# Performance work log

Measured on AMD Instinct MI355X. Metric: run time of the kernel, lower is better.

Reference implementation:

```python
import jax, jax.numpy as jnp
import numpy as np

NUM_EDGE_CLASS = 4
NODE_DIM = 64
BATCH = 8
NUM_NODES = 512


def setup_inputs() -> dict:
    key = jax.random.key(0)
    k1, k2, k3, k4, k5 = jax.random.split(key, 5)
    node_state = jax.random.normal(k1, (BATCH, NUM_NODES, NODE_DIM), dtype=jnp.float32)
    adj_mat = jax.random.randint(k2, (BATCH, NUM_NODES, NUM_NODES), 0, NUM_EDGE_CLASS, dtype=jnp.int32)
    matrix_in = jax.random.normal(k3, (NUM_EDGE_CLASS, NODE_DIM, NODE_DIM), dtype=jnp.float32) * 0.1
    matrix_out = jax.random.normal(k4, (NUM_EDGE_CLASS, NODE_DIM, NODE_DIM), dtype=jnp.float32) * 0.1
    bias = jax.random.normal(k5, (2 * NODE_DIM,), dtype=jnp.float32) * 0.1
    return {"node_state": node_state, "adj_mat": adj_mat,
            "matrix_in": matrix_in, "matrix_out": matrix_out, "bias": bias}


def reference(node_state, adj_mat, matrix_in, matrix_out, bias):
    # Original builds a_in[b,v,w] = matrix_in[adj[b,v,w]] ([B,N,N,D,D]) and a giant
    # [B, N*D, N*D] block matrix; equivalently, with one-hot over edge classes:
    #   msg_in[b,v,d]  = sum_w matrix_in[adj[b,v,w]][d,e]  * h[b,w,e]
    #   msg_out[b,v,d] = sum_w matrix_out[adj[b,w,v]][d,e] * h[b,w,e]  (transposed adj)
    oh = jax.nn.one_hot(adj_mat, matrix_in.shape[0], dtype=node_state.dtype)  # [B,V,W,C]
    msg_in = jnp.einsum('bvwc,cde,bwe->bvd', oh, matrix_in, node_state)
    msg_out = jnp.einsum('bwvc,cde,bwe->bvd', oh, matrix_out, node_state)
    return jnp.concatenate([msg_in, msg_out], axis=-1) + bias  # [B,N,2D]
```

## Files before the change

### kernel.cpp

```cpp
#include <hip/hip_runtime.h>

#define NB 8
#define NN 512
#define DD 64

typedef short bf16x8 __attribute__((ext_vector_type(8)));
typedef float f32x4 __attribute__((ext_vector_type(4)));

__device__ __forceinline__ unsigned short f2bf(float f) {
    unsigned int x = __builtin_bit_cast(unsigned int, f);
    x += 0x7FFFu + ((x >> 16) & 1u);
    return (unsigned short)(x >> 16);
}

__device__ __forceinline__ void gload_lds16(const void* g, void* lds) {
    __builtin_amdgcn_global_load_lds(
        (const __attribute__((address_space(1))) unsigned int*)g,
        (__attribute__((address_space(3))) unsigned int*)lds, 16, 0, 0);
}

__device__ __forceinline__ bf16x8 onehot_packed(unsigned int bits, unsigned int rep) {
    unsigned int x = bits ^ rep;
    unsigned int y = x | (x >> 1);
    unsigned int m = ~y & 0x55555555u;
    union { unsigned int u[4]; bf16x8 v; } r;
    #pragma unroll
    for (int j = 0; j < 4; ++j) {
        unsigned int f = m >> (4 * j);
        r.u[j] = ((f & 1u) ? 0x3F80u : 0u) | ((f & 4u) ? 0x3F800000u : 0u);
    }
    return r.v;
}

__global__ __launch_bounds__(256) void prep_kernel(
    const float* __restrict__ h, const int* __restrict__ adj,
    const float* __restrict__ Min, const float* __restrict__ Mout,
    unsigned int* __restrict__ packR, unsigned int* __restrict__ packC,
    unsigned short* __restrict__ HTbf2, unsigned short* __restrict__ Wbf)
{
    const int blk = blockIdx.x, t = threadIdx.x;
    if (blk < 512) {
        __shared__ int tile[64][65];
        const int b = blk >> 6, ti = blk & 63;
        const int tr = (ti >> 3) * 64, tc = (ti & 7) * 64;
        const int* src = adj + (size_t)b * NN * NN;
        #pragma unroll
        for (int i = 0; i < 16; ++i) {
            int idx = i * 256 + t, rr = idx >> 6, cc = idx & 63;
            tile[rr][cc] = src[(size_t)(tr + rr) * NN + tc + cc];
        }
        __syncthreads();
        {
            int r = t >> 2, g = t & 3;
            unsigned int ur = 0, uc = 0;
            #pragma unroll
            for (int j = 0; j < 16; ++j) {
                ur |= ((unsigned int)tile[r][16 * g + j] & 3u) << (2 * j);
                uc |= ((unsigned int)tile[16 * g + j][r] & 3u) << (2 * j);
            }
            packR[((size_t)b * NN + tr + r) * 32 + (tc >> 4) + g] = ur;
            packC[((size_t)b * NN + tc + r) * 32 + (tr >> 4) + g] = uc;
        }
    } else if (blk < 576) {
        __shared__ float tf[64][65];
        const int bb = blk - 512, b = bb >> 3, w0 = (bb & 7) * 64;
        #pragma unroll
        for (int i = 0; i < 16; ++i) {
            int idx = i * 256 + t, w = idx >> 6, e = idx & 63;
            tf[w][e] = h[((size_t)b * NN + w0 + w) * DD + e];
        }
        __syncthreads();
        unsigned int* HT32 = (unsigned int*)HTbf2;
        const int n = t >> 6, r = (t >> 2) & 15, p = t & 3;
        #pragma unroll
        for (int i = 0; i < 8; ++i) {
            int woct = (w0 >> 3) + i;
            int kb = woct & 3, kc = (woct >> 2) & 3, cch = woct >> 4;
            int slab = (cch * 4 + kc) * 4 + n;
            unsigned int lo = f2bf(tf[8 * i + 2 * p][n * 16 + r]);
            unsigned int hi = f2bf(tf[8 * i + 2 * p + 1][n * 16 + r]);
            HT32[(size_t)b * 16384 + slab * 256 + kb * 64 + r * 4 + p] =
                lo | (hi << 16);
        }
    } else {
        int idx = (blk - 576) * 256 + t;
        int dir = idx >> 14, d = (idx >> 8) & 63, k = idx & 255;
        int c = k >> 6, e = k & 63;
        const float* M = dir ? Mout : Min;
        Wbf[idx] = f2bf(M[(c * DD + d) * DD + e]);
    }
}

__global__ __launch_bounds__(256) void msg_mfma_kernel(
    const unsigned int* __restrict__ packR, const unsigned int* __restrict__ packC,
    const unsigned short* __restrict__ HTbf2, const unsigned short* __restrict__ Wbf,
    const float* __restrict__ bias, float* __restrict__ out)
{
    __shared__ unsigned short HTX[64][512];
    __shared__ unsigned short S2[2][8][256];

    const int t = threadIdx.x;
    const int lane = t & 63, wv = t >> 6;
    const int dir = wv >> 1, rt = wv & 1;
    const int b = blockIdx.x >> 6;
    const int v0 = (blockIdx.x & 63) * 8;
    const int r = lane & 15, kb = lane >> 4;

    const unsigned short* HTg = HTbf2 + (size_t)b * 32768;

    #pragma unroll
    for (int q = 0; q < 16; ++q) {
        int s = wv * 16 + q;
        gload_lds16(HTg + (size_t)s * 512 + lane * 8, &HTX[s][0]);
    }

    const int vloc = rt * 4 + (r >> 2);
    const unsigned int rep = (unsigned int)(r & 3) * 0x55555555u;
    const unsigned short* prow = (const unsigned short*)(
        (dir ? packC : packR) + ((size_t)b * NN + v0 + vloc) * 32);
    unsigned int bits0  = prow[kb];        unsigned int bits1  = prow[4 + kb];
    unsigned int bits2  = prow[8 + kb];    unsigned int bits3  = prow[12 + kb];
    unsigned int bits4  = prow[16 + kb];   unsigned int bits5  = prow[20 + kb];
    unsigned int bits6  = prow[24 + kb];   unsigned int bits7  = prow[28 + kb];
    unsigned int bits8  = prow[32 + kb];   unsigned int bits9  = prow[36 + kb];
    unsigned int bits10 = prow[40 + kb];   unsigned int bits11 = prow[44 + kb];
    unsigned int bits12 = prow[48 + kb];   unsigned int bits13 = prow[52 + kb];
    unsigned int bits14 = prow[56 + kb];   unsigned int bits15 = prow[60 + kb];

    __syncthreads();

    f32x4 acc[4] = {f32x4{0,0,0,0}, f32x4{0,0,0,0}, f32x4{0,0,0,0}, f32x4{0,0,0,0}};
    #pragma unroll
    for (int c = 0; c < 4; ++c) {
        #pragma unroll
        for (int kc = 0; kc < 4; ++kc) {
            unsigned int bits;
            switch (c * 4 + kc) {
                case 0:  bits = bits0;  break;  case 1:  bits = bits1;  break;
                case 2:  bits = bits2;  break;  case 3:  bits = bits3;  break;
                case 4:  bits = bits4;  break;  case 5:  bits = bits5;  break;
                case 6:  bits = bits6;  break;  case 7:  bits = bits7;  break;
                case 8:  bits = bits8;  break;  case 9:  bits = bits9;  break;
                case 10: bits = bits10; break;  case 11: bits = bits11; break;
                case 12: bits = bits12; break;  case 13: bits = bits13; break;
                case 14: bits = bits14; break;  default: bits = bits15; break;
            }
            bf16x8 afrag = onehot_packed(bits, rep);
            #pragma unroll
            for (int n = 0; n < 4; ++n) {
                bf16x8 bfrag = *(const bf16x8*)&HTX[(c * 4 + kc) * 4 + n][lane * 8];
                acc[n] = __builtin_amdgcn_mfma_f32_16x16x32_bf16(afrag, bfrag, acc[n], 0, 0, 0);
            }
        }
    }

    #pragma unroll
    for (int ct = 0; ct < 4; ++ct) {
        #pragma unroll
        for (int rg = 0; rg < 4; ++rg) {
            int row_g = rt * 16 + kb * 4 + rg;
            int vv = row_g >> 2, cc2 = row_g & 3;
            int e = ct * 16 + r;
            int rb = (cc2 * 128 + e * 2) ^ ((vv & 7) << 4);
            *(unsigned short*)((char*)&S2[dir][vv][0] + rb) = f2bf(acc[ct][rg]);
        }
    }
    __syncthreads();

    f32x4 acc2[2] = {f32x4{0,0,0,0}, f32x4{0,0,0,0}};
    #pragma unroll
    for (int kc = 0; kc < 8; ++kc) {
        int vv = r & 7;
        int kbase = kc * 32 + kb * 8;
        int rb = (kbase * 2) ^ (vv << 4);
        bf16x8 a2 = *(const bf16x8*)((const char*)&S2[dir][vv][0] + rb);
        #pragma unroll
        for (int j = 0; j < 2; ++j) {
            int d = (rt * 2 + j) * 16 + r;
            bf16x8 b2 = *(const bf16x8*)&Wbf[(dir * DD + d) * 256 + kbase];
            acc2[j] = __builtin_amdgcn_mfma_f32_16x16x32_bf16(a2, b2, acc2[j], 0, 0, 0);
        }
    }
    #pragma unroll
    for (int j = 0; j < 2; ++j) {
        int d = (rt * 2 + j) * 16 + r;
        float bs = bias[dir * DD + d];
        #pragma unroll
        for (int rg = 0; rg < 4; ++rg) {
            int row = kb * 4 + rg;
            if (row < 8)
                out[((size_t)(b * NN + v0 + row)) * (2 * DD) + dir * DD + d] = acc2[j][rg] + bs;
        }
    }
}

__global__ __launch_bounds__(256) void msg_kernel(
    const float* __restrict__ h, const int* __restrict__ adj,
    const float* __restrict__ Min, const float* __restrict__ Mout,
    const float* __restrict__ bias, float* __restrict__ out)
{
    __shared__ __align__(16) float S[4][2][4][DD];
    const int lane = threadIdx.x & 63, wslot = threadIdx.x >> 6;
    const int wid = blockIdx.x * 4 + wslot;
    const int b = wid >> 9, v = wid & (NN - 1);
    const float* hb = h + (size_t)b * NN * DD;
    const int* adjb = adj + (size_t)b * NN * NN;
    float tot = 0.f, ain1 = 0.f, ain2 = 0.f, ain3 = 0.f, aout1 = 0.f, aout2 = 0.f, aout3 = 0.f;
    for (int w0 = 0; w0 < NN; w0 += 64) {
        int cin_chunk = adjb[v * NN + (w0 + lane)];
        int cout_chunk = adjb[(w0 + lane) * NN + v];
        #pragma unroll
        for (int k = 0; k < 64; ++k) {
            float hw = hb[(w0 + k) * DD + lane];
            int cin = __builtin_amdgcn_readlane(cin_chunk, k);
            int cout = __builtin_amdgcn_readlane(cout_chunk, k);
            tot += hw;
            ain1 = fmaf((cin == 1) ? 1.f : 0.f, hw, ain1);
            ain2 = fmaf((cin == 2) ? 1.f : 0.f, hw, ain2);
            ain3 = fmaf((cin == 3) ? 1.f : 0.f, hw, ain3);
            aout1 = fmaf((cout == 1) ? 1.f : 0.f, hw, aout1);
            aout2 = fmaf((cout == 2) ? 1.f : 0.f, hw, aout2);
            aout3 = fmaf((cout == 3) ? 1.f : 0.f, hw, aout3);
        }
    }
    S[wslot][0][0][lane] = tot - ain1 - ain2 - ain3;
    S[wslot][0][1][lane] = ain1; S[wslot][0][2][lane] = ain2; S[wslot][0][3][lane] = ain3;
    S[wslot][1][0][lane] = tot - aout1 - aout2 - aout3;
    S[wslot][1][1][lane] = aout1; S[wslot][1][2][lane] = aout2; S[wslot][1][3][lane] = aout3;
    __syncthreads();
    float o_in = 0.f, o_out = 0.f;
    #pragma unroll
    for (int c = 0; c < 4; ++c)
        for (int e0 = 0; e0 < DD; e0 += 4) {
            float4 mi = *reinterpret_cast<const float4*>(&Min[(c * DD + lane) * DD + e0]);
            float4 mo = *reinterpret_cast<const float4*>(&Mout[(c * DD + lane) * DD + e0]);
            float4 si = *reinterpret_cast<const float4*>(&S[wslot][0][c][e0]);
            float4 so = *reinterpret_cast<const float4*>(&S[wslot][1][c][e0]);
            o_in = fmaf(mi.x, si.x, fmaf(mi.y, si.y, fmaf(mi.z, si.z, fmaf(mi.w, si.w, o_in))));
            o_out = fmaf(mo.x, so.x, fmaf(mo.y, so.y, fmaf(mo.z, so.z, fmaf(mo.w, so.w, o_out))));
        }
    float* ov = out + (size_t)(b * NN + v) * (2 * DD);
    ov[lane] = o_in + bias[lane];
    ov[DD + lane] = o_out + bias[DD + lane];
}

extern "C" void kernel_launch(void* const* d_in, const int* in_sizes, int n_in,
                              void* d_out, int out_size, void* d_ws, size_t ws_size,
                              hipStream_t stream) {
    const float* node_state = (const float*)d_in[0];
    const int*   adj_mat    = (const int*)  d_in[1];
    const float* matrix_in  = (const float*)d_in[2];
    const float* matrix_out = (const float*)d_in[3];
    const float* bias       = (const float*)d_in[4];
    float* out = (float*)d_out;

    const size_t PACKR_OFF = 0;
    const size_t PACKC_OFF = (size_t)NB * NN * 32 * 4;
    const size_t HT_OFF    = PACKC_OFF + (size_t)NB * NN * 32 * 4;
    const size_t W_OFF     = HT_OFF + (size_t)NB * DD * NN * 2;
    const size_t NEED      = W_OFF + (size_t)2 * DD * 256 * 2;

    if (ws_size < NEED) {
        msg_kernel<<<NB * NN / 4, 256, 0, stream>>>(node_state, adj_mat, matrix_in,
                                                    matrix_out, bias, out);
        return;
    }
    unsigned int*   packR = (unsigned int*)((char*)d_ws + PACKR_OFF);
    unsigned int*   packC = (unsigned int*)((char*)d_ws + PACKC_OFF);
    unsigned short* HTbf2 = (unsigned short*)((char*)d_ws + HT_OFF);
    unsigned short* Wbf   = (unsigned short*)((char*)d_ws + W_OFF);

    prep_kernel<<<704, 256, 0, stream>>>(node_state, adj_mat, matrix_in, matrix_out,
                                         packR, packC, HTbf2, Wbf);
    msg_mfma_kernel<<<NB * NN / 8, 256, 0, stream>>>(packR, packC, HTbf2, Wbf, bias, out);
}
```

Before: 20.16 us.

## Fuse adjacency bit-packing into the MFMA message kernel

```diff
diff --git a/kernel.cpp b/kernel.cpp
--- a/kernel.cpp
+++ b/kernel.cpp
@@ -33,37 +33,14 @@
 }
 
 __global__ __launch_bounds__(256) void prep_kernel(
-    const float* __restrict__ h, const int* __restrict__ adj,
+    const float* __restrict__ h,
     const float* __restrict__ Min, const float* __restrict__ Mout,
-    unsigned int* __restrict__ packR, unsigned int* __restrict__ packC,
     unsigned short* __restrict__ HTbf2, unsigned short* __restrict__ Wbf)
 {
     const int blk = blockIdx.x, t = threadIdx.x;
-    if (blk < 512) {
-        __shared__ int tile[64][65];
-        const int b = blk >> 6, ti = blk & 63;
-        const int tr = (ti >> 3) * 64, tc = (ti & 7) * 64;
-        const int* src = adj + (size_t)b * NN * NN;
-        #pragma unroll
-        for (int i = 0; i < 16; ++i) {
-            int idx = i * 256 + t, rr = idx >> 6, cc = idx & 63;
-            tile[rr][cc] = src[(size_t)(tr + rr) * NN + tc + cc];
-        }
-        __syncthreads();
-        {
-            int r = t >> 2, g = t & 3;
-            unsigned int ur = 0, uc = 0;
-            #pragma unroll
-            for (int j = 0; j < 16; ++j) {
-                ur |= ((unsigned int)tile[r][16 * g + j] & 3u) << (2 * j);
-                uc |= ((unsigned int)tile[16 * g + j][r] & 3u) << (2 * j);
-            }
-            packR[((size_t)b * NN + tr + r) * 32 + (tc >> 4) + g] = ur;
-            packC[((size_t)b * NN + tc + r) * 32 + (tr >> 4) + g] = uc;
-        }
-    } else if (blk < 576) {
+    if (blk < 64) {
         __shared__ float tf[64][65];
-        const int bb = blk - 512, b = bb >> 3, w0 = (bb & 7) * 64;
+        const int b = blk >> 3, w0 = (blk & 7) * 64;
         #pragma unroll
         for (int i = 0; i < 16; ++i) {
             int idx = i * 256 + t, w = idx >> 6, e = idx & 63;
@@ -83,7 +60,7 @@
                 lo | (hi << 16);
         }
     } else {
-        int idx = (blk - 576) * 256 + t;
+        int idx = (blk - 64) * 256 + t;
         int dir = idx >> 14, d = (idx >> 8) & 63, k = idx & 255;
         int c = k >> 6, e = k & 63;
         const float* M = dir ? Mout : Min;
@@ -92,20 +69,23 @@
 }
 
 __global__ __launch_bounds__(256) void msg_mfma_kernel(
-    const unsigned int* __restrict__ packR, const unsigned int* __restrict__ packC,
+    const int* __restrict__ adj,
     const unsigned short* __restrict__ HTbf2, const unsigned short* __restrict__ Wbf,
     const float* __restrict__ bias, float* __restrict__ out)
 {
-    __shared__ unsigned short HTX[64][512];
+    __shared__ __align__(16) unsigned short HTX[64][512];
     __shared__ unsigned short S2[2][8][256];
+    __shared__ __align__(16) unsigned int pR[8][32];
+    __shared__ __align__(16) unsigned int pC[8][32];
 
     const int t = threadIdx.x;
     const int lane = t & 63, wv = t >> 6;
     const int dir = wv >> 1, rt = wv & 1;
-    const int b = blockIdx.x >> 6;
-    const int v0 = (blockIdx.x & 63) * 8;
+    const int b  = blockIdx.x & 7;
+    const int v0 = (blockIdx.x >> 3) * 8;
     const int r = lane & 15, kb = lane >> 4;
 
+    const int* adjb = adj + (size_t)b * NN * NN;
     const unsigned short* HTg = HTbf2 + (size_t)b * 32768;
 
     #pragma unroll
@@ -114,10 +94,46 @@
         gload_lds16(HTg + (size_t)s * 512 + lane * 8, &HTX[s][0]);
     }
 
+    {
+        int v = t >> 5, pk = t & 31;
+        const int* src = adjb + (size_t)(v0 + v) * NN + pk * 16;
+        int4 a0 = *(const int4*)(src + 0),  a1 = *(const int4*)(src + 4);
+        int4 a2 = *(const int4*)(src + 8),  a3 = *(const int4*)(src + 12);
+        unsigned int u =
+            ((unsigned int)a0.x & 3u)        | (((unsigned int)a0.y & 3u) << 2)  |
+            (((unsigned int)a0.z & 3u) << 4) | (((unsigned int)a0.w & 3u) << 6)  |
+            (((unsigned int)a1.x & 3u) << 8) | (((unsigned int)a1.y & 3u) << 10) |
+            (((unsigned int)a1.z & 3u) << 12)| (((unsigned int)a1.w & 3u) << 14) |
+            (((unsigned int)a2.x & 3u) << 16)| (((unsigned int)a2.y & 3u) << 18) |
+            (((unsigned int)a2.z & 3u) << 20)| (((unsigned int)a2.w & 3u) << 22) |
+            (((unsigned int)a3.x & 3u) << 24)| (((unsigned int)a3.y & 3u) << 26) |
+            (((unsigned int)a3.z & 3u) << 28)| (((unsigned int)a3.w & 3u) << 30);
+        pR[v][pk] = u;
+    }
+
+    #pragma unroll
+    for (int it = 0; it < 2; ++it) {
+        int w = it * 256 + t;
+        const int* src = adjb + (size_t)w * NN + v0;
+        int4 a0 = *(const int4*)src, a1 = *(const int4*)(src + 4);
+        int sh = 2 * (w & 15);
+        #pragma unroll
+        for (int v = 0; v < 8; ++v) {
+            int av = (v==0)?a0.x:(v==1)?a0.y:(v==2)?a0.z:(v==3)?a0.w:
+                     (v==4)?a1.x:(v==5)?a1.y:(v==6)?a1.z:a1.w;
+            unsigned int u = ((unsigned int)av & 3u) << sh;
+            u |= __shfl_xor(u, 1);  u |= __shfl_xor(u, 2);
+            u |= __shfl_xor(u, 4);  u |= __shfl_xor(u, 8);
+            if ((t & 15) == v) pC[v][w >> 4] = u;
+        }
+    }
+
+    __syncthreads();
+
     const int vloc = rt * 4 + (r >> 2);
     const unsigned int rep = (unsigned int)(r & 3) * 0x55555555u;
-    const unsigned short* prow = (const unsigned short*)(
-        (dir ? packC : packR) + ((size_t)b * NN + v0 + vloc) * 32);
+    const unsigned short* prow =
+        (const unsigned short*)(dir ? &pC[vloc][0] : &pR[vloc][0]);
     unsigned int bits0  = prow[kb];        unsigned int bits1  = prow[4 + kb];
     unsigned int bits2  = prow[8 + kb];    unsigned int bits3  = prow[12 + kb];
     unsigned int bits4  = prow[16 + kb];   unsigned int bits5  = prow[20 + kb];
@@ -126,8 +142,6 @@
     unsigned int bits10 = prow[40 + kb];   unsigned int bits11 = prow[44 + kb];
     unsigned int bits12 = prow[48 + kb];   unsigned int bits13 = prow[52 + kb];
     unsigned int bits14 = prow[56 + kb];   unsigned int bits15 = prow[60 + kb];
-
-    __syncthreads();
 
     f32x4 acc[4] = {f32x4{0,0,0,0}, f32x4{0,0,0,0}, f32x4{0,0,0,0}, f32x4{0,0,0,0}};
     #pragma unroll
@@ -254,23 +268,19 @@
     const float* bias       = (const float*)d_in[4];
     float* out = (float*)d_out;
 
-    const size_t PACKR_OFF = 0;
-    const size_t PACKC_OFF = (size_t)NB * NN * 32 * 4;
-    const size_t HT_OFF    = PACKC_OFF + (size_t)NB * NN * 32 * 4;
-    const size_t W_OFF     = HT_OFF + (size_t)NB * DD * NN * 2;
-    const size_t NEED      = W_OFF + (size_t)2 * DD * 256 * 2;
+    const size_t HT_OFF = 0;
+    const size_t W_OFF  = (size_t)NB * 32768 * 2;
+    const size_t NEED   = W_OFF + (size_t)2 * DD * 256 * 2;
 
     if (ws_size < NEED) {
         msg_kernel<<<NB * NN / 4, 256, 0, stream>>>(node_state, adj_mat, matrix_in,
                                                     matrix_out, bias, out);
         return;
     }
-    unsigned int*   packR = (unsigned int*)((char*)d_ws + PACKR_OFF);
-    unsigned int*   packC = (unsigned int*)((char*)d_ws + PACKC_OFF);
     unsigned short* HTbf2 = (unsigned short*)((char*)d_ws + HT_OFF);
     unsigned short* Wbf   = (unsigned short*)((char*)d_ws + W_OFF);
 
-    prep_kernel<<<704, 256, 0, stream>>>(node_state, adj_mat, matrix_in, matrix_out,
-                                         packR, packC, HTbf2, Wbf);
-    msg_mfma_kernel<<<NB * NN / 8, 256, 0, stream>>>(packR, packC, HTbf2, Wbf, bias, out);
-}
+    prep_kernel<<<192, 256, 0, stream>>>(node_state, matrix_in, matrix_out,
+                                         HTbf2, Wbf);
+    msg_mfma_kernel<<<NB * NN / 8, 256, 0, stream>>>(adj_mat, HTbf2, Wbf, bias, out);
+}
```

Result: slower. 22.71 us (+12.7%).
